# Kernel tuning notes

Measured on AMD Instinct MI355X. Metric: run time of the kernel, lower is better.

## Reference

```python
import jax, jax.numpy as jnp
import numpy as np
import math

WINDOW = 512
N_HEAD = 16

def setup_inputs() -> dict:
    key = jax.random.key(0)
    ks = jax.random.split(key, 5)
    B, L, D = 2, 4096, 1024
    s = 0.02
    return {
        "x": jax.random.normal(ks[0], (B, L, D), dtype=jnp.float32),
        "Wq": jax.random.normal(ks[1], (D, D), dtype=jnp.float32) * s,
        "bq": jnp.zeros((D,), jnp.float32),
        "Wk": jax.random.normal(ks[2], (D, D), dtype=jnp.float32) * s,
        "bk": jnp.zeros((D,), jnp.float32),
        "Wv": jax.random.normal(ks[3], (D, D), dtype=jnp.float32) * s,
        "bv": jnp.zeros((D,), jnp.float32),
        "Wo": jax.random.normal(ks[4], (D, D), dtype=jnp.float32) * s,
        "bo": jnp.zeros((D,), jnp.float32),
    }

def reference(x, Wq, bq, Wk, bk, Wv, bv, Wo, bo):
    # Chunked sliding-window MHA (eval mode, dropout inactive).
    B, L, D = x.shape
    W, H = WINDOW, N_HEAD
    dh = D // H
    C = L // W  # number of query chunks
    scale = 1.0 / math.sqrt(dh)

    # Project full sequence once (linear, per-token -> identical math).
    q = x @ Wq.T + bq
    k = x @ Wk.T + bk
    v = x @ Wv.T + bv

    # Pad K/V by one window at the front so every chunk sees 2W keys.
    kp = jnp.pad(k, ((0, 0), (W, 0), (0, 0)))
    vp = jnp.pad(v, ((0, 0), (W, 0), (0, 0)))
    idx = jnp.arange(C)[:, None] * W + jnp.arange(2 * W)[None, :]  # [C, 2W] into padded seq
    kc = kp[:, idx].reshape(B, C, 2 * W, H, dh)
    vc = vp[:, idx].reshape(B, C, 2 * W, H, dh)
    qc = q.reshape(B, C, W, H, dh)

    scores = jnp.einsum('bcqhd,bckhd->bchqk', qc, kc) * scale  # [B,C,H,W,2W]
    valid = (idx >= W)  # padded positions (chunk 0's lookback) are invalid
    scores = jnp.where(valid[None, :, None, None, :], scores, jnp.float32(-1e9))
    attn = jax.nn.softmax(scores, axis=-1)
    out = jnp.einsum('bchqk,bckhd->bcqhd', attn, vc).reshape(B, L, D)
    return out @ Wo.T + bo
```

## Files before the change

kernel.cpp:

```cpp
#include <hip/hip_runtime.h>
#include <hip/hip_bf16.h>

typedef __hip_bfloat16 bf16;
typedef __attribute__((ext_vector_type(8))) short bf16x8;
typedef __attribute__((ext_vector_type(4))) float f32x4;
typedef unsigned int u32;
typedef unsigned short u16;

#define MFMA(a,b,c) __builtin_amdgcn_mfma_f32_16x16x32_bf16((a),(b),(c),0,0,0)

__device__ __forceinline__ u16 f32_to_bf16_rtne(float f) {
  u32 b = __builtin_bit_cast(u32, f);
  b += 0x7FFFu + ((b >> 16) & 1u);
  return (u16)(b >> 16);
}
__device__ __forceinline__ u32 pk2bf(float a, float b) {
  u32 ua = __builtin_bit_cast(u32, a); ua += 0x7FFFu + ((ua >> 16) & 1u);
  u32 ub = __builtin_bit_cast(u32, b); ub += 0x7FFFu + ((ub >> 16) & 1u);
  return __builtin_amdgcn_perm(ub, ua, 0x07060302u);
}
__device__ __forceinline__ u32 pk2bf_rtz(float a, float b) {
  return __builtin_amdgcn_perm(__builtin_bit_cast(u32, b),
                               __builtin_bit_cast(u32, a), 0x07060302u);
}
__device__ __forceinline__ uint4 cvt8(uint4 lo, uint4 hi) {
  const float4 fl = __builtin_bit_cast(float4, lo);
  const float4 fh = __builtin_bit_cast(float4, hi);
  uint4 r;
  r.x = pk2bf(fl.x, fl.y); r.y = pk2bf(fl.z, fl.w);
  r.z = pk2bf(fh.x, fh.y); r.w = pk2bf(fh.z, fh.w);
  return r;
}

__device__ __forceinline__ void barrier_lgkm() {
  asm volatile("s_waitcnt lgkmcnt(0)\n\ts_barrier" ::: "memory");
}

static constexpr float SL2E = 0.125f * 1.44269504f;

__global__ __launch_bounds__(256)
void cast_w(const float* __restrict__ wq, const float* __restrict__ wk,
            const float* __restrict__ wv, const float* __restrict__ wo,
            u16* __restrict__ wqkv, u16* __restrict__ wob) {
  const size_t DD8 = (size_t)1024 * 1024 / 8;
  const int m = blockIdx.x >> 9;
  const size_t i = ((size_t)(blockIdx.x & 511)) * 256 + threadIdx.x;
  const float* src = (m == 0) ? wq : (m == 1) ? wk : (m == 2) ? wv : wo;
  u16* dst = (m < 3) ? (wqkv + (size_t)m * DD8 * 8) : wob;
  const float4* s = (const float4*)src + i * 2;
  uint4 v = cvt8(__builtin_bit_cast(uint4, s[0]), __builtin_bit_cast(uint4, s[1]));
  ((uint4*)dst)[i] = v;
}

template <int MODE, int CASTA>
__global__ __launch_bounds__(256)
void gemm_bt(const void* __restrict__ Asrc, const bf16* __restrict__ W,
             const float* __restrict__ b0, const float* __restrict__ b1,
             const float* __restrict__ b2, void* __restrict__ o0,
             void* __restrict__ o1, void* __restrict__ o2,
             int M, int N, int K)
{
  __shared__ bf16 As[128 * 64];
  __shared__ bf16 Bs[128 * 64];

  const int tid  = threadIdx.x;
  const int wave = tid >> 6, lane = tid & 63;
  const int quad = lane >> 4, l16 = lane & 15;
  const int wm   = wave >> 1, wn  = wave & 1;
  const int m0   = blockIdx.x * 128, n0 = blockIdx.y * 128;

  const int band = n0 >> 10;
  const float* bias = (band == 0) ? b0 : (band == 1) ? b1 : b2;

  const int srow = lane >> 3;
  const int sg   = lane & 7;
  const size_t rgs = (size_t)8 * K;
  const bf16*  aSrcH = (const bf16*)Asrc  + (size_t)(m0 + wave * 32 + srow) * K + sg * 8;
  const float* aSrcF = (const float*)Asrc + (size_t)(m0 + wave * 32 + srow) * K + sg * 8;
  const bf16*  wSrc  = W + (size_t)(n0 + wave * 32 + srow) * K + sg * 8;
  bf16* aDst = As + (wave * 32 + srow) * 64 + ((sg ^ srow) * 8);
  bf16* wDst = Bs + (wave * 32 + srow) * 64 + ((sg ^ srow) * 8);

  const int niter = K >> 6;

  uint4 a0, a1, a2, a3;
  uint4 a0h, a1h, a2h, a3h;
  if (CASTA) {
    a0 = *(const uint4*)(aSrcF);            a0h = *(const uint4*)(aSrcF + 4);
    a1 = *(const uint4*)(aSrcF + rgs);      a1h = *(const uint4*)(aSrcF + rgs + 4);
    a2 = *(const uint4*)(aSrcF + 2 * rgs);  a2h = *(const uint4*)(aSrcF + 2 * rgs + 4);
    a3 = *(const uint4*)(aSrcF + 3 * rgs);  a3h = *(const uint4*)(aSrcF + 3 * rgs + 4);
    aSrcF += 64;
  } else {
    a0 = *(const uint4*)(aSrcH);
    a1 = *(const uint4*)(aSrcH + rgs);
    a2 = *(const uint4*)(aSrcH + 2 * rgs);
    a3 = *(const uint4*)(aSrcH + 3 * rgs);
    aSrcH += 64;
  }
  uint4 w0 = *(const uint4*)(wSrc);
  uint4 w1 = *(const uint4*)(wSrc + rgs);
  uint4 w2 = *(const uint4*)(wSrc + 2 * rgs);
  uint4 w3 = *(const uint4*)(wSrc + 3 * rgs);
  wSrc += 64;

  f32x4 acc[4][4] = {};

  const int arow[4] = { (wm * 64 + 0 * 16 + l16) * 64, (wm * 64 + 1 * 16 + l16) * 64,
                        (wm * 64 + 2 * 16 + l16) * 64, (wm * 64 + 3 * 16 + l16) * 64 };
  const int brow[4] = { (wn * 64 + 0 * 16 + l16) * 64, (wn * 64 + 1 * 16 + l16) * 64,
                        (wn * 64 + 2 * 16 + l16) * 64, (wn * 64 + 3 * 16 + l16) * 64 };
  const int r7 = l16 & 7;

  for (int t = 0; t < niter; ++t) {
    if (t) barrier_lgkm();
    if (CASTA) {
      *(uint4*)(aDst)        = cvt8(a0, a0h);
      *(uint4*)(aDst + 512)  = cvt8(a1, a1h);
      *(uint4*)(aDst + 1024) = cvt8(a2, a2h);
      *(uint4*)(aDst + 1536) = cvt8(a3, a3h);
    } else {
      *(uint4*)(aDst)        = a0;
      *(uint4*)(aDst + 512)  = a1;
      *(uint4*)(aDst + 1024) = a2;
      *(uint4*)(aDst + 1536) = a3;
    }
    *(uint4*)(wDst)        = w0;
    *(uint4*)(wDst + 512)  = w1;
    *(uint4*)(wDst + 1024) = w2;
    *(uint4*)(wDst + 1536) = w3;
    barrier_lgkm();
    if (t + 1 < niter) {
      if (CASTA) {
        a0 = *(const uint4*)(aSrcF);            a0h = *(const uint4*)(aSrcF + 4);
        a1 = *(const uint4*)(aSrcF + rgs);      a1h = *(const uint4*)(aSrcF + rgs + 4);
        a2 = *(const uint4*)(aSrcF + 2 * rgs);  a2h = *(const uint4*)(aSrcF + 2 * rgs + 4);
        a3 = *(const uint4*)(aSrcF + 3 * rgs);  a3h = *(const uint4*)(aSrcF + 3 * rgs + 4);
        aSrcF += 64;
      } else {
        a0 = *(const uint4*)(aSrcH);
        a1 = *(const uint4*)(aSrcH + rgs);
        a2 = *(const uint4*)(aSrcH + 2 * rgs);
        a3 = *(const uint4*)(aSrcH + 3 * rgs);
        aSrcH += 64;
      }
      w0 = *(const uint4*)(wSrc);
      w1 = *(const uint4*)(wSrc + rgs);
      w2 = *(const uint4*)(wSrc + 2 * rgs);
      w3 = *(const uint4*)(wSrc + 3 * rgs);
      wSrc += 64;
    }
#pragma unroll
    for (int kk = 0; kk < 2; ++kk) {
      bf16x8 af[4], bw[4];
#pragma unroll
      for (int mt = 0; mt < 4; ++mt)
        af[mt] = *(const bf16x8*)(As + arow[mt] + (((kk * 4 + quad) ^ r7) * 8));
#pragma unroll
      for (int nt = 0; nt < 4; ++nt)
        bw[nt] = *(const bf16x8*)(Bs + brow[nt] + (((kk * 4 + quad) ^ r7) * 8));
#pragma unroll
      for (int mt = 0; mt < 4; ++mt)
#pragma unroll
        for (int nt = 0; nt < 4; ++nt)
          acc[mt][nt] = MFMA(af[mt], bw[nt], acc[mt][nt]);
    }
  }

#pragma unroll
  for (int nt = 0; nt < 4; ++nt) {
    const int col = n0 + wn * 64 + nt * 16 + l16;
    const int cl  = col & 1023;
    const float bv = bias[cl];
#pragma unroll
    for (int mt = 0; mt < 4; ++mt) {
      const int rbase = m0 + wm * 64 + mt * 16 + quad * 4;
      if (MODE == 1) {
#pragma unroll
        for (int r = 0; r < 4; ++r)
          ((float*)o0)[(size_t)(rbase + r) * N + col] = acc[mt][nt][r] + bv;
      } else if (band == 2) {
        const int hh = cl >> 6, dd = cl & 63;
        const int bb = rbase >> 12, tl = rbase & 4095;
        u16* dst = (u16*)o2 + ((size_t)((bb * 16 + hh) * 64 + dd)) * 4096 + tl;
        uint2 pk;
        pk.x = pk2bf(acc[mt][nt][0] + bv, acc[mt][nt][1] + bv);
        pk.y = pk2bf(acc[mt][nt][2] + bv, acc[mt][nt][3] + bv);
        *(uint2*)dst = pk;
      } else {
        u16* dst = (u16*)((band == 0) ? o0 : o1);
        const float sc = (band == 0) ? SL2E : 1.0f;
#pragma unroll
        for (int r = 0; r < 4; ++r)
          dst[(size_t)(rbase + r) * 1024 + cl] =
              f32_to_bf16_rtne((acc[mt][nt][r] + bv) * sc);
      }
    }
  }
}

__global__ __launch_bounds__(256)
void attn_swin(const bf16* __restrict__ qb, const bf16* __restrict__ kb,
               const bf16* __restrict__ vtb, u16* __restrict__ ctx)
{
  __shared__ __align__(16) bf16 Ks[2][64 * 72];
  __shared__ __align__(16) bf16 Vts[2][64 * 72];

  int bid = blockIdx.x;
  const int g  = bid & 255, qt = bid >> 8;
  const int h  = g & 15, c = (g >> 4) & 7, b = g >> 7;

  const int tid  = threadIdx.x;
  const int w    = tid >> 6, lane = tid & 63;
  const int quad = lane >> 4, l16 = lane & 15;

  const int tq0  = c * 512 + qt * 128;
  const int hoff = h * 64;
  const int kstart = (c == 0) ? 0 : (c - 1) * 512;
  const int nkt    = (c == 0) ? 8 : 16;

  bf16x8 qf[2][2];
#pragma unroll
  for (int u = 0; u < 2; ++u) {
    const bf16* qr = qb + ((size_t)(b * 4096 + tq0 + w * 32 + u * 16 + l16)) * 1024 + hoff;
    qf[u][0] = *(const bf16x8*)(qr + quad * 8);
    qf[u][1] = *(const bf16x8*)(qr + 32 + quad * 8);
  }

  const int m    = tid >> 2;
  const int cseg = (tid & 3) * 16;
  const int sig  = (((m >> 4) & 1) << 5) | (((m >> 2) & 3) << 3)
                 | (((m >> 5) & 1) << 2) | (m & 3);
  const bf16* kgp = kb + ((size_t)(b * 4096 + kstart + sig)) * 1024 + hoff + cseg;
  const bf16* vgp = vtb + ((size_t)((b * 16 + h) * 64 + m)) * 4096 + kstart + cseg;
  const int soff = m * 72 + cseg;

  float l_i[2] = {0.f, 0.f};
  f32x4 o[2][4] = {};

  uint4 ka0 = *(const uint4*)(kgp), ka1 = *(const uint4*)(kgp + 8);
  uint4 va0 = *(const uint4*)(vgp), va1 = *(const uint4*)(vgp + 8);
  kgp += (size_t)64 * 1024; vgp += 64;
  *(uint4*)(Ks[0] + soff) = ka0; *(uint4*)(Ks[0] + soff + 8) = ka1;
  *(uint4*)(Vts[0] + soff) = va0; *(uint4*)(Vts[0] + soff + 8) = va1;
  ka0 = *(const uint4*)(kgp); ka1 = *(const uint4*)(kgp + 8);
  va0 = *(const uint4*)(vgp); va1 = *(const uint4*)(vgp + 8);
  kgp += (size_t)64 * 1024; vgp += 64;
  barrier_lgkm();

  typedef union { u32 d[4]; bf16x8 v; } fragu;

  auto compute = [&](const bf16* ksb, const bf16* vtsb) {
    f32x4 s[2][4] = {};
#pragma unroll
    for (int kt = 0; kt < 4; ++kt) {
      const bf16* kr = ksb + (kt * 16 + l16) * 72;
      bf16x8 kf0 = *(const bf16x8*)(kr + quad * 8);
      bf16x8 kf1 = *(const bf16x8*)(kr + 32 + quad * 8);
      s[0][kt] = MFMA(kf0, qf[0][0], s[0][kt]);
      s[0][kt] = MFMA(kf1, qf[0][1], s[0][kt]);
      s[1][kt] = MFMA(kf0, qf[1][0], s[1][kt]);
      s[1][kt] = MFMA(kf1, qf[1][1], s[1][kt]);
    }
    fragu pf[2][2];
#pragma unroll
    for (int u = 0; u < 2; ++u) {
      float rs = 0.f;
#pragma unroll
      for (int kt = 0; kt < 4; ++kt)
#pragma unroll
        for (int r = 0; r < 4; ++r) {
          const float p = __builtin_amdgcn_exp2f(s[u][kt][r]);
          s[u][kt][r] = p;
          rs += p;
        }
      rs += __shfl_xor(rs, 16);
      rs += __shfl_xor(rs, 32);
      l_i[u] += rs;
#pragma unroll
      for (int hh = 0; hh < 2; ++hh)
#pragma unroll
        for (int dw = 0; dw < 4; ++dw) {
          const int kt = 2 * (dw >> 1) + hh, r0 = 2 * (dw & 1);
          pf[u][hh].d[dw] = pk2bf_rtz(s[u][kt][r0], s[u][kt][r0 + 1]);
        }
    }
#pragma unroll
    for (int dt = 0; dt < 4; ++dt) {
      const bf16* vr = vtsb + (dt * 16 + l16) * 72;
      bf16x8 vf0 = *(const bf16x8*)(vr + quad * 8);
      bf16x8 vf1 = *(const bf16x8*)(vr + 32 + quad * 8);
      o[0][dt] = MFMA(vf0, pf[0][0].v, o[0][dt]);
      o[0][dt] = MFMA(vf1, pf[0][1].v, o[0][dt]);
      o[1][dt] = MFMA(vf0, pf[1][0].v, o[1][dt]);
      o[1][dt] = MFMA(vf1, pf[1][1].v, o[1][dt]);
    }
  };

  for (int t = 0; t < nkt; t += 2) {
    *(uint4*)(Ks[1] + soff) = ka0; *(uint4*)(Ks[1] + soff + 8) = ka1;
    *(uint4*)(Vts[1] + soff) = va0; *(uint4*)(Vts[1] + soff + 8) = va1;
    if (t + 2 < nkt) {
      ka0 = *(const uint4*)(kgp); ka1 = *(const uint4*)(kgp + 8);
      va0 = *(const uint4*)(vgp); va1 = *(const uint4*)(vgp + 8);
      kgp += (size_t)64 * 1024; vgp += 64;
    }
    compute(Ks[0], Vts[0]);
    barrier_lgkm();

    if (t + 2 < nkt) {
      *(uint4*)(Ks[0] + soff) = ka0; *(uint4*)(Ks[0] + soff + 8) = ka1;
      *(uint4*)(Vts[0] + soff) = va0; *(uint4*)(Vts[0] + soff + 8) = va1;
      if (t + 3 < nkt) {
        ka0 = *(const uint4*)(kgp); ka1 = *(const uint4*)(kgp + 8);
        va0 = *(const uint4*)(vgp); va1 = *(const uint4*)(vgp + 8);
        kgp += (size_t)64 * 1024; vgp += 64;
      }
    }
    compute(Ks[1], Vts[1]);
    barrier_lgkm();
  }

#pragma unroll
  for (int u = 0; u < 2; ++u) {
    const float inv = 1.0f / l_i[u];
    const int qrow = tq0 + w * 32 + u * 16 + l16;
    u16* crow = ctx + ((size_t)(b * 4096 + qrow)) * 1024 + hoff;
#pragma unroll
    for (int dt = 0; dt < 4; ++dt) {
      uint2 pk;
      pk.x = pk2bf(o[u][dt][0] * inv, o[u][dt][1] * inv);
      pk.y = pk2bf(o[u][dt][2] * inv, o[u][dt][3] * inv);
      *(uint2*)(crow + dt * 16 + quad * 4) = pk;
    }
  }
}

extern "C" void kernel_launch(void* const* d_in, const int* in_sizes, int n_in,
                              void* d_out, int out_size, void* d_ws, size_t ws_size,
                              hipStream_t stream) {
  const float* x  = (const float*)d_in[0];
  const float* Wq = (const float*)d_in[1];
  const float* bq = (const float*)d_in[2];
  const float* Wk = (const float*)d_in[3];
  const float* bk = (const float*)d_in[4];
  const float* Wv = (const float*)d_in[5];
  const float* bv = (const float*)d_in[6];
  const float* Wo = (const float*)d_in[7];
  const float* bo = (const float*)d_in[8];

  const size_t MD = (size_t)8192 * 1024;
  const size_t DD = (size_t)1024 * 1024;

  char* ws = (char*)d_ws;
  u16*  Wqkvb = (u16*)ws;                     ws += 3 * DD * 2;
  u16*  Wob   = (u16*)ws;                     ws += DD * 2;
  u16*  qbuf  = (u16*)ws;                     ws += MD * 2;
  u16*  kbuf  = (u16*)ws;                     ws += MD * 2;
  u16*  vtb   = (u16*)ws;                     ws += MD * 2;
  u16*  ctx   = (u16*)ws;

  cast_w<<<dim3(2048), dim3(256), 0, stream>>>(Wq, Wk, Wv, Wo, Wqkvb, Wob);

  gemm_bt<0, 1><<<dim3(64, 24), dim3(256), 0, stream>>>(
      x, (const bf16*)Wqkvb, bq, bk, bv, qbuf, kbuf, vtb, 8192, 3072, 1024);

  attn_swin<<<dim3(1024), dim3(256), 0, stream>>>(
      (const bf16*)qbuf, (const bf16*)kbuf, (const bf16*)vtb, ctx);

  gemm_bt<1, 0><<<dim3(64, 8), dim3(256), 0, stream>>>(
      ctx, (const bf16*)Wob, bo, bo, bo, d_out, nullptr, nullptr, 8192, 1024, 1024);
}
```

Before: 241.5 us.

## Pre-cast x to bf16 and use direct global-to-LDS loads in GEMM

The fp32-to-bf16 conversion of x moves out of the QKV GEMM into the existing weight-cast kernel, writing into the ctx buffer, which is reused later. The GEMM then drops its register-staged prefetch and stores in favour of global_load_lds 16-byte loads straight into swizzled LDS, with the swizzle applied on the source address. This removes register pressure and the VGPR-to-LDS store path. It loses the software prefetch overlap, since loads are now issued and waited on within each iteration without double buffering, and it adds an extra pass over x in memory.

```diff
diff --git a/kernel.cpp b/kernel.cpp
--- a/kernel.cpp
+++ b/kernel.cpp
@@ -36,25 +36,40 @@
   asm volatile("s_waitcnt lgkmcnt(0)\n\ts_barrier" ::: "memory");
 }
 
+typedef const __attribute__((address_space(1))) void* gas_ptr;
+typedef __attribute__((address_space(3))) void* las_ptr;
+__device__ __forceinline__ void gload_lds16(const void* g, void* l) {
+  __builtin_amdgcn_global_load_lds((gas_ptr)g, (las_ptr)l, 16, 0, 0);
+}
+
 static constexpr float SL2E = 0.125f * 1.44269504f;
 
 __global__ __launch_bounds__(256)
-void cast_w(const float* __restrict__ wq, const float* __restrict__ wk,
-            const float* __restrict__ wv, const float* __restrict__ wo,
-            u16* __restrict__ wqkv, u16* __restrict__ wob) {
+void cast_all(const float* __restrict__ wq, const float* __restrict__ wk,
+              const float* __restrict__ wv, const float* __restrict__ wo,
+              const float* __restrict__ x,
+              u16* __restrict__ wqkv, u16* __restrict__ wob,
+              u16* __restrict__ xb) {
   const size_t DD8 = (size_t)1024 * 1024 / 8;
-  const int m = blockIdx.x >> 9;
-  const size_t i = ((size_t)(blockIdx.x & 511)) * 256 + threadIdx.x;
-  const float* src = (m == 0) ? wq : (m == 1) ? wk : (m == 2) ? wv : wo;
-  u16* dst = (m < 3) ? (wqkv + (size_t)m * DD8 * 8) : wob;
-  const float4* s = (const float4*)src + i * 2;
-  uint4 v = cvt8(__builtin_bit_cast(uint4, s[0]), __builtin_bit_cast(uint4, s[1]));
-  ((uint4*)dst)[i] = v;
-}
-
-template <int MODE, int CASTA>
+  if (blockIdx.x < 2048) {
+    const int m = blockIdx.x >> 9;
+    const size_t i = ((size_t)(blockIdx.x & 511)) * 256 + threadIdx.x;
+    const float* src = (m == 0) ? wq : (m == 1) ? wk : (m == 2) ? wv : wo;
+    u16* dst = (m < 3) ? (wqkv + (size_t)m * DD8 * 8) : wob;
+    const float4* s = (const float4*)src + i * 2;
+    ((uint4*)dst)[i] = cvt8(__builtin_bit_cast(uint4, s[0]),
+                            __builtin_bit_cast(uint4, s[1]));
+  } else {
+    const size_t i = ((size_t)(blockIdx.x - 2048)) * 256 + threadIdx.x;
+    const float4* s = (const float4*)x + i * 2;
+    ((uint4*)xb)[i] = cvt8(__builtin_bit_cast(uint4, s[0]),
+                           __builtin_bit_cast(uint4, s[1]));
+  }
+}
+
+template <int MODE>
 __global__ __launch_bounds__(256)
-void gemm_bt(const void* __restrict__ Asrc, const bf16* __restrict__ W,
+void gemm_bt(const bf16* __restrict__ A, const bf16* __restrict__ W,
              const float* __restrict__ b0, const float* __restrict__ b1,
              const float* __restrict__ b2, void* __restrict__ o0,
              void* __restrict__ o1, void* __restrict__ o2,
@@ -75,34 +90,12 @@
   const int srow = lane >> 3;
   const int sg   = lane & 7;
   const size_t rgs = (size_t)8 * K;
-  const bf16*  aSrcH = (const bf16*)Asrc  + (size_t)(m0 + wave * 32 + srow) * K + sg * 8;
-  const float* aSrcF = (const float*)Asrc + (size_t)(m0 + wave * 32 + srow) * K + sg * 8;
-  const bf16*  wSrc  = W + (size_t)(n0 + wave * 32 + srow) * K + sg * 8;
-  bf16* aDst = As + (wave * 32 + srow) * 64 + ((sg ^ srow) * 8);
-  bf16* wDst = Bs + (wave * 32 + srow) * 64 + ((sg ^ srow) * 8);
+  const bf16* aSrc = A + (size_t)(m0 + wave * 32 + srow) * K + ((sg ^ srow) * 8);
+  const bf16* wSrc = W + (size_t)(n0 + wave * 32 + srow) * K + ((sg ^ srow) * 8);
+  bf16* aB = As + wave * 32 * 64;
+  bf16* wB = Bs + wave * 32 * 64;
 
   const int niter = K >> 6;
-
-  uint4 a0, a1, a2, a3;
-  uint4 a0h, a1h, a2h, a3h;
-  if (CASTA) {
-    a0 = *(const uint4*)(aSrcF);            a0h = *(const uint4*)(aSrcF + 4);
-    a1 = *(const uint4*)(aSrcF + rgs);      a1h = *(const uint4*)(aSrcF + rgs + 4);
-    a2 = *(const uint4*)(aSrcF + 2 * rgs);  a2h = *(const uint4*)(aSrcF + 2 * rgs + 4);
-    a3 = *(const uint4*)(aSrcF + 3 * rgs);  a3h = *(const uint4*)(aSrcF + 3 * rgs + 4);
-    aSrcF += 64;
-  } else {
-    a0 = *(const uint4*)(aSrcH);
-    a1 = *(const uint4*)(aSrcH + rgs);
-    a2 = *(const uint4*)(aSrcH + 2 * rgs);
-    a3 = *(const uint4*)(aSrcH + 3 * rgs);
-    aSrcH += 64;
-  }
-  uint4 w0 = *(const uint4*)(wSrc);
-  uint4 w1 = *(const uint4*)(wSrc + rgs);
-  uint4 w2 = *(const uint4*)(wSrc + 2 * rgs);
-  uint4 w3 = *(const uint4*)(wSrc + 3 * rgs);
-  wSrc += 64;
 
   f32x4 acc[4][4] = {};
 
@@ -113,43 +106,17 @@
   const int r7 = l16 & 7;
 
   for (int t = 0; t < niter; ++t) {
-    if (t) barrier_lgkm();
-    if (CASTA) {
-      *(uint4*)(aDst)        = cvt8(a0, a0h);
-      *(uint4*)(aDst + 512)  = cvt8(a1, a1h);
-      *(uint4*)(aDst + 1024) = cvt8(a2, a2h);
-      *(uint4*)(aDst + 1536) = cvt8(a3, a3h);
-    } else {
-      *(uint4*)(aDst)        = a0;
-      *(uint4*)(aDst + 512)  = a1;
-      *(uint4*)(aDst + 1024) = a2;
-      *(uint4*)(aDst + 1536) = a3;
-    }
-    *(uint4*)(wDst)        = w0;
-    *(uint4*)(wDst + 512)  = w1;
-    *(uint4*)(wDst + 1024) = w2;
-    *(uint4*)(wDst + 1536) = w3;
-    barrier_lgkm();
-    if (t + 1 < niter) {
-      if (CASTA) {
-        a0 = *(const uint4*)(aSrcF);            a0h = *(const uint4*)(aSrcF + 4);
-        a1 = *(const uint4*)(aSrcF + rgs);      a1h = *(const uint4*)(aSrcF + rgs + 4);
-        a2 = *(const uint4*)(aSrcF + 2 * rgs);  a2h = *(const uint4*)(aSrcF + 2 * rgs + 4);
-        a3 = *(const uint4*)(aSrcF + 3 * rgs);  a3h = *(const uint4*)(aSrcF + 3 * rgs + 4);
-        aSrcF += 64;
-      } else {
-        a0 = *(const uint4*)(aSrcH);
-        a1 = *(const uint4*)(aSrcH + rgs);
-        a2 = *(const uint4*)(aSrcH + 2 * rgs);
-        a3 = *(const uint4*)(aSrcH + 3 * rgs);
-        aSrcH += 64;
-      }
-      w0 = *(const uint4*)(wSrc);
-      w1 = *(const uint4*)(wSrc + rgs);
-      w2 = *(const uint4*)(wSrc + 2 * rgs);
-      w3 = *(const uint4*)(wSrc + 3 * rgs);
-      wSrc += 64;
-    }
+    gload_lds16(aSrc,            aB);
+    gload_lds16(aSrc + rgs,      aB + 512);
+    gload_lds16(aSrc + 2 * rgs,  aB + 1024);
+    gload_lds16(aSrc + 3 * rgs,  aB + 1536);
+    gload_lds16(wSrc,            wB);
+    gload_lds16(wSrc + rgs,      wB + 512);
+    gload_lds16(wSrc + 2 * rgs,  wB + 1024);
+    gload_lds16(wSrc + 3 * rgs,  wB + 1536);
+    aSrc += 64; wSrc += 64;
+    __syncthreads();
+
 #pragma unroll
     for (int kk = 0; kk < 2; ++kk) {
       bf16x8 af[4], bw[4];
@@ -165,6 +132,7 @@
         for (int nt = 0; nt < 4; ++nt)
           acc[mt][nt] = MFMA(af[mt], bw[nt], acc[mt][nt]);
     }
+    if (t + 1 < niter) __syncthreads();
   }
 
 #pragma unroll
@@ -360,14 +328,19 @@
   u16*  vtb   = (u16*)ws;                     ws += MD * 2;
   u16*  ctx   = (u16*)ws;
 
-  cast_w<<<dim3(2048), dim3(256), 0, stream>>>(Wq, Wk, Wv, Wo, Wqkvb, Wob);
-
-  gemm_bt<0, 1><<<dim3(64, 24), dim3(256), 0, stream>>>(
-      x, (const bf16*)Wqkvb, bq, bk, bv, qbuf, kbuf, vtb, 8192, 3072, 1024);
+  u16* xb = ctx;
+
+  cast_all<<<dim3(6144), dim3(256), 0, stream>>>(Wq, Wk, Wv, Wo, x,
+                                                 Wqkvb, Wob, xb);
+
+  gemm_bt<0><<<dim3(64, 24), dim3(256), 0, stream>>>(
+      (const bf16*)xb, (const bf16*)Wqkvb, bq, bk, bv,
+      qbuf, kbuf, vtb, 8192, 3072, 1024);
 
   attn_swin<<<dim3(1024), dim3(256), 0, stream>>>(
       (const bf16*)qbuf, (const bf16*)kbuf, (const bf16*)vtb, ctx);
 
-  gemm_bt<1, 0><<<dim3(64, 8), dim3(256), 0, stream>>>(
-      ctx, (const bf16*)Wob, bo, bo, bo, d_out, nullptr, nullptr, 8192, 1024, 1024);
-}
+  gemm_bt<1><<<dim3(64, 8), dim3(256), 0, stream>>>(
+      (const bf16*)ctx, (const bf16*)Wob, bo, bo, bo,
+      d_out, nullptr, nullptr, 8192, 1024, 1024);
+}
```

Result: no change. 240.0 us (-0.6%).
